# Kernel tuning notes

Hardware: AMD Instinct MI355X
Metric: run time of the kernel (lower is better)

Reference implementation:

```python
import jax, jax.numpy as jnp
import numpy as np

H = 1024      # hidden_size
NH = 16       # num_heads
HD = H // NH  # head_dim


def setup_inputs() -> dict:
    key = jax.random.key(0)
    ks = jax.random.split(key, 12)
    inp = {
        "query": jax.random.normal(ks[0], (4, 1024, H), dtype=jnp.float32),
        "key": jax.random.normal(ks[1], (4, 2048, H), dtype=jnp.float32),
        "value": jax.random.normal(ks[2], (4, 2048, H), dtype=jnp.float32),
        "key_padding_mask": jax.random.randint(ks[3], (4, 2048), 0, 2, dtype=jnp.int32),
        # learned parameters (torch Linear: y = x @ W.T + b); we store W already transposed
        "Wq": jax.random.normal(ks[4], (H, H), dtype=jnp.float32) * (1.0 / np.sqrt(H)),
        "bq": jnp.zeros((H,), dtype=jnp.float32),
        "Wk": jax.random.normal(ks[5], (H, H), dtype=jnp.float32) * (1.0 / np.sqrt(H)),
        "bk": jnp.zeros((H,), dtype=jnp.float32),
        "Wv": jax.random.normal(ks[6], (H, H), dtype=jnp.float32) * (1.0 / np.sqrt(H)),
        "bv": jnp.zeros((H,), dtype=jnp.float32),
        "Wo": jax.random.normal(ks[7], (H, H), dtype=jnp.float32) * (1.0 / np.sqrt(H)),
        "bo": jnp.zeros((H,), dtype=jnp.float32),
    }
    return inp


def reference(query, key, value, key_padding_mask, Wq, bq, Wk, bk, Wv, bv, Wo, bo):
    B, Sq, _ = query.shape
    Sk = key.shape[1]
    scaling = HD ** -0.5
    # projections -> [B, NH, S, HD]
    q = (query @ Wq + bq).reshape(B, Sq, NH, HD).transpose(0, 2, 1, 3)
    k = (key @ Wk + bk).reshape(B, Sk, NH, HD).transpose(0, 2, 1, 3)
    v = (value @ Wv + bv).reshape(B, Sk, NH, HD).transpose(0, 2, 1, 3)
    # scores [B, NH, Sq, Sk]
    scores = jnp.einsum("bhqd,bhkd->bhqk", q, k) * scaling
    # mask: positions where key_padding_mask == 0 are ignored
    scores = jnp.where((key_padding_mask == 0)[:, None, None, :], -jnp.inf, scores)
    attn = jax.nn.softmax(scores, axis=-1)
    # dropout is identity in eval mode
    out = jnp.einsum("bhqk,bhkd->bhqd", attn, v)
    out = out.transpose(0, 2, 1, 3).reshape(B, Sq, H)
    return out @ Wo + bo
```

## Files before the change

### kernel.cpp

```cpp
#include <hip/hip_runtime.h>
#include <hip/hip_fp16.h>
#include <math.h>

#define B_ 4
#define SQ 1024
#define SK 2048
#define HH 1024
#define NHEAD 16
#define HDIM 64

typedef _Float16 f16;
typedef __attribute__((ext_vector_type(8))) _Float16 f16x8;
typedef __attribute__((ext_vector_type(4))) _Float16 f16x4;
typedef __attribute__((ext_vector_type(4))) float f32x4;
typedef unsigned int u32;

#define GLOAD_LDS16(gp, lp) __builtin_amdgcn_global_load_lds( \
    (const __attribute__((address_space(1))) u32*)(gp),        \
    (__attribute__((address_space(3))) u32*)(lp), 16, 0, 0)
#define GLOAD_LDS4(gp, lp) __builtin_amdgcn_global_load_lds(  \
    (const __attribute__((address_space(1))) u32*)(gp),        \
    (__attribute__((address_space(3))) u32*)(lp), 4, 0, 0)

__global__ __launch_bounds__(256) void prep_k(
    const float* __restrict__ W0, const float* __restrict__ W1,
    const float* __restrict__ W2, const float* __restrict__ W3,
    const int* __restrict__ mask,
    f16* __restrict__ WT, float* __restrict__ pbias)
{
    __shared__ f16 t[64 * 80];
    const int bid = blockIdx.x, tid = threadIdx.x;
    if (bid < 1024) {
        int z = bid >> 8, idx = bid & 255;
        const float* W = z == 0 ? W0 : z == 1 ? W1 : z == 2 ? W2 : W3;
        f16* out = WT + (size_t)z * HH * HH;
        const int r0 = (idx >> 4) * 64, c0 = (idx & 15) * 64;
#pragma unroll
        for (int p = 0; p < 4; p++) {
            int s = p * 256 + tid;
            int row = s >> 4, u = s & 15;
            float4 a = *(const float4*)(W + (size_t)(r0 + row) * HH + c0 + u * 4);
            f16x4 vv;
            vv[0] = (f16)a.x; vv[1] = (f16)a.y; vv[2] = (f16)a.z; vv[3] = (f16)a.w;
            *(f16x4*)(t + row * 80 + u * 4) = vv;
        }
        __syncthreads();
#pragma unroll
        for (int p = 0; p < 2; p++) {
            int s = p * 256 + tid;
            int n = s >> 3, u = s & 7;
            f16x8 vv;
#pragma unroll
            for (int j = 0; j < 8; j++) vv[j] = t[(u * 8 + j) * 80 + n];
            *(f16x8*)(out + (size_t)(c0 + n) * HH + r0 + u * 8) = vv;
        }
    } else {
        int j = (bid - 1024) * 256 + tid;
        pbias[j] = mask[j] ? 0.f : -1e30f;
    }
}

template <int TM, int OUTMODE, int CASTA>
__device__ __forceinline__ void gemm_body(
    const void* Ain, const f16* __restrict__ BT,
    const float* __restrict__ bias, void* __restrict__ Cout,
    int bid, int nwg, f16* sA, f16* sB)
{
    const int tid = threadIdx.x, lane = tid & 63, w = tid >> 6;
    const int swz = (bid & 7) * (nwg >> 3) + (bid >> 3);
    const int m0 = (swz >> 3) * TM;
    const int n0 = (swz & 7) * 128;
    const int wr = w >> 1, wc = w & 1;
    const int ql = lane & 15, g = lane >> 4;
    const int N = 1024, K = 1024;
    const int MF = TM / 32;
    const int ABUF = TM * 32;
    const int NP = TM / 64;
    f32x4 acc[MF][4] = {};

    const float* A32 = (const float*)Ain;
    const f16*   A16 = (const f16*)Ain;

    auto stageB = [&](int buf, int k0) {
#pragma unroll
        for (int p = 0; p < 2; p++) {
            int s = p * 256 + tid;
            int row = s >> 2, us = ((s & 3) ^ ((row >> 1) & 3)) * 8;
            GLOAD_LDS16(BT + (size_t)(n0 + row) * K + k0 + us,
                        sB + buf * 4096 + (p * 256 + w * 64) * 8);
        }
    };
    auto loadA = [&](int k0, float4* r) {
#pragma unroll
        for (int p = 0; p < NP; p++) {
            int s = p * 256 + tid;
            int row = s >> 2, u = s & 3;
            const float* ap = A32 + (size_t)(m0 + row) * K + k0 + u * 8;
            r[2 * p]     = *(const float4*)ap;
            r[2 * p + 1] = *(const float4*)(ap + 4);
        }
    };
    auto writeA = [&](int buf, const float4* r) {
#pragma unroll
        for (int p = 0; p < NP; p++) {
            int s = p * 256 + tid;
            int row = s >> 2, u = s & 3;
            float4 a0 = r[2 * p], a1 = r[2 * p + 1];
            f16x8 v;
            v[0] = (f16)a0.x; v[1] = (f16)a0.y; v[2] = (f16)a0.z; v[3] = (f16)a0.w;
            v[4] = (f16)a1.x; v[5] = (f16)a1.y; v[6] = (f16)a1.z; v[7] = (f16)a1.w;
            *(f16x8*)(sA + buf * ABUF + row * 32 + ((u ^ ((row >> 1) & 3)) * 8)) = v;
        }
    };
    auto stageA16 = [&](int buf, int k0) {
#pragma unroll
        for (int p = 0; p < NP; p++) {
            int s = p * 256 + tid;
            int row = s >> 2, us = ((s & 3) ^ ((row >> 1) & 3)) * 8;
            GLOAD_LDS16(A16 + (size_t)(m0 + row) * K + k0 + us,
                        sA + buf * ABUF + (p * 256 + w * 64) * 8);
        }
    };
    auto compute = [&](int buf) {
        f16x8 af[MF], bf[4];
#pragma unroll
        for (int m = 0; m < MF; m++) {
            int row = wr * (TM / 2) + m * 16 + ql;
            af[m] = *(const f16x8*)(sA + buf * ABUF + row * 32 + ((g ^ ((row >> 1) & 3)) * 8));
        }
#pragma unroll
        for (int n = 0; n < 4; n++) {
            int row = wc * 64 + n * 16 + ql;
            bf[n] = *(const f16x8*)(sB + buf * 4096 + row * 32 + ((g ^ ((row >> 1) & 3)) * 8));
        }
#pragma unroll
        for (int m = 0; m < MF; m++)
#pragma unroll
            for (int n = 0; n < 4; n++)
                acc[m][n] = __builtin_amdgcn_mfma_f32_16x16x32_f16(af[m], bf[n], acc[m][n], 0, 0, 0);
    };

    if (CASTA) {
        float4 r0[2 * NP], r1[2 * NP];
        loadA(0, r0);
        stageB(0, 0);
        writeA(0, r0);
        loadA(32, r0);
#pragma unroll 1
        for (int k0 = 0; k0 < K; k0 += 64) {
            __syncthreads();
            stageB(1, k0 + 32);
            if (k0 + 64 < K) loadA(k0 + 64, r1);
            compute(0);
            writeA(1, r0);
            __syncthreads();
            if (k0 + 64 < K) {
                stageB(0, k0 + 64);
                if (k0 + 96 < K) loadA(k0 + 96, r0);
            }
            compute(1);
            if (k0 + 64 < K) writeA(0, r1);
        }
    } else {
        stageA16(0, 0);
        stageB(0, 0);
        int cur = 0;
#pragma unroll 1
        for (int k0 = 0; k0 < K; k0 += 32) {
            __syncthreads();
            if (k0 + 32 < K) { stageA16(cur ^ 1, k0 + 32); stageB(cur ^ 1, k0 + 32); }
            compute(cur);
            cur ^= 1;
        }
    }

    float bv[4];
#pragma unroll
    for (int n = 0; n < 4; n++) bv[n] = bias[n0 + wc * 64 + n * 16 + ql];
#pragma unroll
    for (int m = 0; m < MF; m++) {
        int row0 = m0 + wr * (TM / 2) + m * 16 + g * 4;
#pragma unroll
        for (int n = 0; n < 4; n++) {
            int col = n0 + wc * 64 + n * 16 + ql;
            if (OUTMODE == 2) {
                int bb = row0 >> 11, kk = row0 & 2047;
                int hh = col >> 6, dd = col & 63;
                f16x4 vv;
#pragma unroll
                for (int e = 0; e < 4; e++) vv[e] = (f16)(acc[m][n][e] + bv[n]);
                *(f16x4*)((f16*)Cout + ((size_t)(bb * NHEAD + hh) * HDIM + dd) * SK + kk) = vv;
            } else if (OUTMODE == 1) {
#pragma unroll
                for (int e = 0; e < 4; e++)
                    ((f16*)Cout)[(size_t)(row0 + e) * N + col] = (f16)(acc[m][n][e] + bv[n]);
            } else {
#pragma unroll
                for (int e = 0; e < 4; e++)
                    ((float*)Cout)[(size_t)(row0 + e) * N + col] = acc[m][n][e] + bv[n];
            }
        }
    }
}

__global__ __launch_bounds__(256, 3) void qkv_gemm_k(
    const float* __restrict__ q, const float* __restrict__ k,
    const float* __restrict__ v, const f16* __restrict__ wT,
    const float* __restrict__ bq, const float* __restrict__ bk,
    const float* __restrict__ bv,
    f16* __restrict__ qp, f16* __restrict__ kp, f16* __restrict__ vt)
{
    __shared__ f16 sA[2 * 4096];
    __shared__ f16 sB[2 * 4096];
    const int bid = blockIdx.x;
    const size_t M1 = 1024 * 1024;
    if (bid < 512)
        gemm_body<64, 1, 1>(q, wT, bq, qp, bid, 512, sA, sB);
    else if (bid < 1024)
        gemm_body<128, 1, 1>(k, wT + M1, bk, kp, bid - 512, 512, sA, sB);
    else
        gemm_body<128, 2, 1>(v, wT + 2 * M1, bv, vt, bid - 1024, 512, sA, sB);
}

__global__ __launch_bounds__(256) void o_gemm_k(
    const f16* __restrict__ ctx, const f16* __restrict__ wT,
    const float* __restrict__ bo, float* __restrict__ out)
{
    __shared__ f16 sA[2 * 4096];
    __shared__ f16 sB[2 * 4096];
    gemm_body<64, 0, 0>(ctx, wT, bo, out, blockIdx.x, 512, sA, sB);
}

#define SC2 0.18033688f
#define THR2 11.5f

__global__ __launch_bounds__(512, 4) void attn_mfma_k(
    const f16* __restrict__ qp,
    const f16* __restrict__ kp,
    const f16* __restrict__ vt,
    const float* __restrict__ pbias,
    f16* __restrict__ ctx)
{
    const int flat = ((int)blockIdx.x & 7) * 64 + ((int)blockIdx.x >> 3);
    const int qt = flat & 7, h = (flat >> 3) & 15, b = flat >> 7;
    const int q0 = qt * 128;
    const int tid = threadIdx.x, lane = tid & 63, w = tid >> 6;
    const int ql = lane & 15, g = lane >> 4;

    __shared__ f16 ks[2 * 4096];
    __shared__ f16 vs[2 * 4096];
    __shared__ f16 plds[8][16 * 64];
    __shared__ float sbias[2][64];

    const f16* kbase = kp + (size_t)b * SK * HH + h * HDIM;
    const f16* vbase = vt + ((size_t)(b * NHEAD + h)) * HDIM * SK;
    const float* bbase = pbias + b * SK;

    f16x8 qf[2];
    {
        const f16* qb = qp + ((size_t)(b * SQ + q0 + w * 16 + ql)) * HH + h * HDIM + g * 8;
        qf[0] = *(const f16x8*)qb;
        qf[1] = *(const f16x8*)(qb + 32);
    }

    auto stageKV = [&](int buf, int kt) {
        int r = tid >> 3, ulg = ((tid & 7) ^ (r & 7)) * 8;
        GLOAD_LDS16(kbase + (size_t)(kt + r) * HH + ulg, ks + buf * 4096 + w * 512);
        GLOAD_LDS16(vbase + (size_t)r * SK + kt + ulg,   vs + buf * 4096 + w * 512);
        if (w == 0) GLOAD_LDS4(bbase + kt + lane, &sbias[buf][0]);
    };

    f32x4 oacc[4] = {};
    float mrun = -1e30f, lrun = 0.f;
    f16* pw = &plds[w][0];

    auto tile = [&](const f16* kb, const f16* vb, const float* sb,
                    bool pf_en, int pbuf, int pkt) {
        __syncthreads();
        if (pf_en) stageKV(pbuf, pkt);

        f32x4 sacc[4] = {};
        __builtin_amdgcn_s_setprio(1);
#pragma unroll
        for (int n = 0; n < 4; n++) {
            int key = n * 16 + ql;
#pragma unroll
            for (int df = 0; df < 2; df++) {
                int u = df * 4 + g;
                f16x8 kf = *(const f16x8*)(kb + key * 64 + ((u ^ (key & 7)) * 8));
                sacc[n] = __builtin_amdgcn_mfma_f32_16x16x32_f16(kf, qf[df], sacc[n], 0, 0, 0);
            }
        }
        __builtin_amdgcn_s_setprio(0);

        float sv[4][4];
        float mt = -1e30f;
#pragma unroll
        for (int n = 0; n < 4; n++) {
            float4 b4 = *(const float4*)&sb[n * 16 + g * 4];
            float barr[4] = {b4.x, b4.y, b4.z, b4.w};
#pragma unroll
            for (int e = 0; e < 4; e++) {
                float s = fmaf(sacc[n][e], SC2, barr[e]);
                sv[n][e] = s;
                mt = fmaxf(mt, s);
            }
        }
        mt = fmaxf(mt, __shfl_xor(mt, 16, 64));
        mt = fmaxf(mt, __shfl_xor(mt, 32, 64));

        if (__any(mt > mrun + THR2)) {
            float mnew = fmaxf(mrun, mt);
            float alpha = __builtin_amdgcn_exp2f(mrun - mnew);
            mrun = mnew;
            lrun *= alpha;
            float al[4];
#pragma unroll
            for (int e = 0; e < 4; e++) al[e] = __shfl(alpha, g * 4 + e, 64);
#pragma unroll
            for (int df = 0; df < 4; df++)
#pragma unroll
                for (int e = 0; e < 4; e++) oacc[df][e] *= al[e];
        }

        float tsum = 0.f;
#pragma unroll
        for (int n = 0; n < 4; n++) {
            float p0 = __builtin_amdgcn_exp2f(sv[n][0] - mrun);
            float p1 = __builtin_amdgcn_exp2f(sv[n][1] - mrun);
            float p2 = __builtin_amdgcn_exp2f(sv[n][2] - mrun);
            float p3 = __builtin_amdgcn_exp2f(sv[n][3] - mrun);
            tsum += (p0 + p1) + (p2 + p3);
            f16x4 pv4;
            pv4[0] = (f16)p0; pv4[1] = (f16)p1; pv4[2] = (f16)p2; pv4[3] = (f16)p3;
            *(f16x4*)(pw + ql * 64 + (((2 * n + (g >> 1)) ^ (ql & 7)) * 8) + (g & 1) * 4) = pv4;
        }
        tsum += __shfl_xor(tsum, 16, 64);
        tsum += __shfl_xor(tsum, 32, 64);
        lrun += tsum;

        __builtin_amdgcn_s_setprio(1);
#pragma unroll
        for (int t = 0; t < 2; t++) {
            f16x8 pf = *(const f16x8*)(pw + ql * 64 + (((t * 4 + g) ^ (ql & 7)) * 8));
#pragma unroll
            for (int df = 0; df < 4; df++) {
                int d = df * 16 + ql;
                int u = t * 4 + g;
                f16x8 vf = *(const f16x8*)(vb + d * 64 + ((u ^ (d & 7)) * 8));
                oacc[df] = __builtin_amdgcn_mfma_f32_16x16x32_f16(pf, vf, oacc[df], 0, 0, 0);
            }
        }
        __builtin_amdgcn_s_setprio(0);
    };

    stageKV(0, 0);
#pragma unroll 1
    for (int kt = 0; kt < SK; kt += 128) {
        tile(ks, vs, sbias[0], true, 1, kt + 64);
        tile(ks + 4096, vs + 4096, sbias[1], kt + 128 < SK, 0, kt + 128);
    }

    float linv[4];
#pragma unroll
    for (int e = 0; e < 4; e++) {
        float lv = __shfl(lrun, g * 4 + e, 64);
        linv[e] = 1.f / lv;
    }
    f16* ob = ctx + ((size_t)(b * SQ + q0 + w * 16)) * HH + h * HDIM;
#pragma unroll
    for (int df = 0; df < 4; df++)
#pragma unroll
        for (int e = 0; e < 4; e++)
            ob[(size_t)(g * 4 + e) * HH + df * 16 + ql] = (f16)(oacc[df][e] * linv[e]);
}

extern "C" void kernel_launch(void* const* d_in, const int* in_sizes, int n_in,
                              void* d_out, int out_size, void* d_ws, size_t ws_size,
                              hipStream_t stream) {
    const float* query = (const float*)d_in[0];
    const float* key   = (const float*)d_in[1];
    const float* value = (const float*)d_in[2];
    const int*   mask  = (const int*)d_in[3];
    const float* Wq = (const float*)d_in[4];
    const float* bq = (const float*)d_in[5];
    const float* Wk = (const float*)d_in[6];
    const float* bk = (const float*)d_in[7];
    const float* Wv = (const float*)d_in[8];
    const float* bv = (const float*)d_in[9];
    const float* Wo = (const float*)d_in[10];
    const float* bo = (const float*)d_in[11];
    float* out = (float*)d_out;

    const size_t M1 = 1024 * 1024;
    f16* wT    = (f16*)d_ws;
    f16* qp    = wT + 4 * M1;
    f16* kp    = qp + 4 * M1;
    f16* vt    = kp + 8 * M1;
    f16* ctx   = vt + 8 * M1;
    float* pbias = (float*)(ctx + 4 * M1);

    dim3 blk(256);

    prep_k<<<dim3(1056), blk, 0, stream>>>(Wq, Wk, Wv, Wo, mask, wT, pbias);

    qkv_gemm_k<<<dim3(1536), blk, 0, stream>>>(query, key, value, wT,
                                               bq, bk, bv, qp, kp, vt);

    attn_mfma_k<<<dim3(512), dim3(512), 0, stream>>>(qp, kp, vt, pbias, ctx);

    o_gemm_k<<<dim3(512), blk, 0, stream>>>(ctx, wT + 3 * M1, bo, out);
}
```

Measured before the change: 154.8 us.

## Use explicit vmcnt/lgkmcnt waits and barriers in QKV GEMM cast pipeline

Replaces __syncthreads in the fp32-cast A path of the GEMM mainloop with hand-placed s_waitcnt vmcnt/lgkmcnt and raw s_barrier, peeling the last iteration so the loop has no conditionals. The intent is to let outstanding global loads for the next stage stay in flight across barriers instead of draining all memory counters. It also raises the launch-bounds occupancy hint from 3 to 4 waves per SIMD, which may force register spilling. The loop bound is hardcoded to K=1024, and the vmcnt constants depend on the exact per-thread load count.

```diff
diff --git a/kernel.cpp b/kernel.cpp
--- a/kernel.cpp
+++ b/kernel.cpp
@@ -21,6 +21,10 @@
 #define GLOAD_LDS4(gp, lp) __builtin_amdgcn_global_load_lds(  \
     (const __attribute__((address_space(1))) u32*)(gp),        \
     (__attribute__((address_space(3))) u32*)(lp), 4, 0, 0)
+
+#define VMWAIT(N) asm volatile("s_waitcnt vmcnt(" #N ")" ::: "memory")
+#define LGKM0     asm volatile("s_waitcnt lgkmcnt(0)" ::: "memory")
+#define BAR()     __builtin_amdgcn_s_barrier()
 
 __global__ __launch_bounds__(256) void prep_k(
     const float* __restrict__ W0, const float* __restrict__ W1,
@@ -141,26 +145,34 @@
     };
 
     if (CASTA) {
-        float4 r0[2 * NP], r1[2 * NP];
-        loadA(0, r0);
+        float4 rE[2 * NP], rO[2 * NP];
         stageB(0, 0);
-        writeA(0, r0);
-        loadA(32, r0);
+        loadA(0, rE);
+        VMWAIT(0);
+        writeA(0, rE);
+        loadA(32, rE);
+        LGKM0; BAR();
 #pragma unroll 1
-        for (int k0 = 0; k0 < K; k0 += 64) {
-            __syncthreads();
+        for (int k0 = 0; k0 < 960; k0 += 64) {
             stageB(1, k0 + 32);
-            if (k0 + 64 < K) loadA(k0 + 64, r1);
+            loadA(k0 + 64, rO);
             compute(0);
-            writeA(1, r0);
-            __syncthreads();
-            if (k0 + 64 < K) {
-                stageB(0, k0 + 64);
-                if (k0 + 96 < K) loadA(k0 + 96, r0);
-            }
+            if constexpr (TM == 128) VMWAIT(4); else VMWAIT(2);
+            writeA(1, rE);
+            LGKM0; BAR();
+            stageB(0, k0 + 64);
+            loadA(k0 + 96, rE);
             compute(1);
-            if (k0 + 64 < K) writeA(0, r1);
-        }
+            if constexpr (TM == 128) VMWAIT(4); else VMWAIT(2);
+            writeA(0, rO);
+            LGKM0; BAR();
+        }
+        stageB(1, 992);
+        compute(0);
+        VMWAIT(0);
+        writeA(1, rE);
+        LGKM0; BAR();
+        compute(1);
     } else {
         stageA16(0, 0);
         stageB(0, 0);
@@ -203,7 +215,7 @@
     }
 }
 
-__global__ __launch_bounds__(256, 3) void qkv_gemm_k(
+__global__ __launch_bounds__(256, 4) void qkv_gemm_k(
     const float* __restrict__ q, const float* __restrict__ k,
     const float* __restrict__ v, const f16* __restrict__ wT,
     const float* __restrict__ bq, const float* __restrict__ bk,
```

Measured after the change: 187.3 us. +21.0%, slower.
